# Optimization experiments

Hardware: AMD Instinct MI355X
Metric: run time of the kernel (lower is better)

The kernel has to match this reference:

```python
import jax, jax.numpy as jnp
import numpy as np

BATCH = 2048
SEQ_LEN = 8192


def setup_inputs() -> dict:
    key = jax.random.key(0)
    k1, k2 = jax.random.split(key)
    inputs = jax.random.normal(k1, (BATCH, SEQ_LEN), dtype=jnp.float32)
    filters = jax.random.normal(k2, (BATCH, SEQ_LEN), dtype=jnp.float32)
    return {"inputs": inputs, "filters": filters}


def reference(inputs, filters):
    # FFT-based long convolution with zero-padding to 2L (linear, not circular, conv).
    # torch norm='forward': rfft divides by n, irfft multiplies by n -> net scale 1/n.
    L = inputs.shape[-1]
    n = 2 * L  # rfft with n=2L implicitly zero-pads, same as F.pad then rfft
    x_f = jnp.fft.rfft(inputs, n=n, axis=-1, norm="forward")   # (B, L+1) complex
    h_f = jnp.fft.rfft(filters, n=n, axis=-1, norm="forward")  # (B, L+1) complex
    y = jnp.fft.irfft(x_f * h_f, n=n, axis=-1, norm="forward")  # (B, 2L)
    return y[..., :L]
```

## Files before the change

kernel.cpp:

```cpp
#include <hip/hip_runtime.h>

#define L_LEN 8192
#define N_FFT 16384
#define NB    1024

#define LB __launch_bounds__(NB)

typedef float f2 __attribute__((ext_vector_type(2)));

__device__ __forceinline__ f2 mkf2(float a, float b) { f2 v; v.x = a; v.y = b; return v; }

__device__ __forceinline__ f2 cmul(f2 a, f2 w) {
    return mkf2(a.y, a.y) * mkf2(-w.y, w.x) + mkf2(a.x, a.x) * w;
}

__host__ __device__ constexpr int swz(int i) {
    return i ^ ((((i) >> 4) ^ ((i) >> 8) ^ ((i) >> 12)) & 15);
}

__device__ __forceinline__ int rev4_12(int m) {
    int r = 0;
#pragma unroll
    for (int d = 0; d < 6; ++d) { r = (r << 2) | (m & 3); m >>= 2; }
    return r;
}

__device__ __forceinline__ void bfly_dif(f2& x0, f2& x1, f2& x2, f2& x3,
                                         f2 w1, f2 w2, f2 w3) {
    f2 A = x0 + x2, B = x0 - x2, C = x1 + x3, D = x1 - x3;
    f2 iD = mkf2(-D.y, D.x);
    x0 = A + C;
    x1 = cmul(B - iD, w1);
    x2 = cmul(A - C, w2);
    x3 = cmul(B + iD, w3);
}

__device__ __forceinline__ void bfly_dit(f2& x0, f2& x1, f2& x2, f2& x3,
                                         f2 w1, f2 w2, f2 w3) {
    f2 a1 = cmul(x1, w1), a2 = cmul(x2, w2), a3 = cmul(x3, w3);
    f2 E = x0 + a2, F = x0 - a2, G = a1 + a3, K = a1 - a3;
    f2 iK = mkf2(-K.y, K.x);
    x0 = E + G; x1 = F + iK; x2 = E - G; x3 = F - iK;
}

__device__ __forceinline__ void bfly_dif1(f2* z) {
    f2 A = z[0] + z[2], B = z[0] - z[2], C = z[1] + z[3], D = z[1] - z[3];
    f2 iD = mkf2(-D.y, D.x);
    z[0] = A + C; z[1] = B - iD; z[2] = A - C; z[3] = B + iD;
}
__device__ __forceinline__ void bfly_dit1(f2* z) {
    f2 E = z[0] + z[2], F = z[0] - z[2], G = z[1] + z[3], K = z[1] - z[3];
    f2 iK = mkf2(-K.y, K.x);
    z[0] = E + G; z[1] = F + iK; z[2] = E - G; z[3] = F - iK;
}

__device__ __forceinline__ void pointwise_pair(f2& Zm, f2& Zr) {
    f2 half = mkf2(0.5f, 0.5f);
    f2 X = half * (Zm + mkf2(Zr.x, -Zr.y));
    f2 H = half * (mkf2(Zm.y, -Zm.x) + mkf2(Zr.y, Zr.x));
    f2 Y = cmul(X, H);
    Zm = Y;
    Zr = mkf2(Y.x, -Y.y);
}

#define CT0 1.0f
#define CT1 0.92387953251128674f
#define CT2 0.70710678118654752f
#define CT3 0.38268343236508977f
#define ST1 0.38268343236508977f
#define ST2 0.70710678118654752f
#define ST3 0.92387953251128674f

template<int QA>
__device__ __forceinline__ void fwd_pair(f2* lds, int tid) {
    constexpr int QB = QA / 4;
    const int g = tid / QB;
    const int u = tid % QB;
    const int sb = swz(g * (4 * QA) + u);
    f2 r[4][4];
#pragma unroll
    for (int jA = 0; jA < 4; ++jA)
#pragma unroll
        for (int jB = 0; jB < 4; ++jB)
            r[jA][jB] = lds[sb ^ swz(jA * QA + jB * QB)];

    {
        const float angA = -6.283185307179586f / (float)(4 * QA);
        float sn, cs;
        __sincosf(angA * (float)u, &sn, &cs);
        f2 u1 = mkf2(cs, sn);
        const f2 lad[4] = {mkf2(CT0, 0.f), mkf2(CT1, -ST1), mkf2(CT2, -ST2), mkf2(CT3, -ST3)};
#pragma unroll
        for (int jB = 0; jB < 4; ++jB) {
            f2 w1 = (jB == 0) ? u1 : cmul(u1, lad[jB]);
            f2 w2 = cmul(w1, w1);
            f2 w3 = cmul(w2, w1);
            bfly_dif(r[0][jB], r[1][jB], r[2][jB], r[3][jB], w1, w2, w3);
        }
    }
    {
        const float angB = -6.283185307179586f / (float)(4 * QB);
        float sn, cs;
        __sincosf(angB * (float)u, &sn, &cs);
        f2 v1 = mkf2(cs, sn);
        f2 v2 = cmul(v1, v1);
        f2 v3 = cmul(v2, v1);
#pragma unroll
        for (int jA = 0; jA < 4; ++jA)
            bfly_dif(r[jA][0], r[jA][1], r[jA][2], r[jA][3], v1, v2, v3);
    }

#pragma unroll
    for (int jA = 0; jA < 4; ++jA)
#pragma unroll
        for (int jB = 0; jB < 4; ++jB)
            lds[sb ^ swz(jA * QA + jB * QB)] = r[jA][jB];
}

template<int QA>
__device__ __forceinline__ void inv_pair(f2* lds, int tid) {
    constexpr int QB = 4 * QA;
    const int G = tid / QA;
    const int u = tid % QA;
    const int sb = swz(G * (16 * QA) + u);
    f2 r[4][4];
#pragma unroll
    for (int jA = 0; jA < 4; ++jA)
#pragma unroll
        for (int jB = 0; jB < 4; ++jB)
            r[jA][jB] = lds[sb ^ swz(jA * QA + jB * QB)];

    {
        const float angA = 6.283185307179586f / (float)(4 * QA);
        float sn, cs;
        __sincosf(angA * (float)u, &sn, &cs);
        f2 a1 = mkf2(cs, sn);
        f2 a2 = cmul(a1, a1);
        f2 a3 = cmul(a2, a1);
#pragma unroll
        for (int jB = 0; jB < 4; ++jB)
            bfly_dit(r[0][jB], r[1][jB], r[2][jB], r[3][jB], a1, a2, a3);
    }
    {
        const float angB = 6.283185307179586f / (float)(4 * QB);
        float sn, cs;
        __sincosf(angB * (float)u, &sn, &cs);
        f2 b1 = mkf2(cs, sn);
        const f2 lad[4] = {mkf2(CT0, 0.f), mkf2(CT1, ST1), mkf2(CT2, ST2), mkf2(CT3, ST3)};
#pragma unroll
        for (int jA = 0; jA < 4; ++jA) {
            f2 w1 = (jA == 0) ? b1 : cmul(b1, lad[jA]);
            f2 w2 = cmul(w1, w1);
            f2 w3 = cmul(w2, w1);
            bfly_dit(r[jA][0], r[jA][1], r[jA][2], r[jA][3], w1, w2, w3);
        }
    }

#pragma unroll
    for (int jA = 0; jA < 4; ++jA)
#pragma unroll
        for (int jB = 0; jB < 4; ++jB)
            lds[sb ^ swz(jA * QA + jB * QB)] = r[jA][jB];
}

__global__ LB
void fftconv_kernel(const float* __restrict__ xin,
                    const float* __restrict__ hin,
                    float* __restrict__ out)
{
    __shared__ f2 lds[N_FFT];

    const int row = blockIdx.x;
    const int tid = threadIdx.x;
    const float* xr = xin + (size_t)row * L_LEN;
    const float* hr = hin + (size_t)row * L_LEN;

    const int s4t = swz(4 * tid);
#pragma unroll
    for (int iter = 0; iter < 2; ++iter) {
        float4 xv = ((const float4*)xr)[tid + iter * NB];
        float4 hv = ((const float4*)hr)[tid + iter * NB];
        lds[s4t ^ swz(iter * 4096 + 0)] = mkf2(xv.x, hv.x);
        lds[s4t ^ swz(iter * 4096 + 1)] = mkf2(xv.y, hv.y);
        lds[s4t ^ swz(iter * 4096 + 2)] = mkf2(xv.z, hv.z);
        lds[s4t ^ swz(iter * 4096 + 3)] = mkf2(xv.w, hv.w);
    }
    const int st = swz(tid);
#pragma unroll
    for (int it = 0; it < 8; ++it)
        lds[st ^ swz(8192 + it * 1024)] = mkf2(0.f, 0.f);
    __syncthreads();

    fwd_pair<4096>(lds, tid); __syncthreads();
    fwd_pair<256>(lds, tid);  __syncthreads();
    fwd_pair<16>(lds, tid);   __syncthreads();

#pragma unroll
    for (int iter = 0; iter < 2; ++iter) {
        const int p = tid + iter * NB;
        if (p == 0) {
            f2 z[4];
#pragma unroll
            for (int k = 0; k < 4; ++k) z[k] = lds[k];
            bfly_dif1(z);
            z[0] = mkf2(z[0].x * z[0].y, 0.f);
            z[2] = mkf2(z[2].x * z[2].y, 0.f);
            pointwise_pair(z[1], z[3]);
            bfly_dit1(z);
#pragma unroll
            for (int k = 0; k < 4; ++k) lds[k] = z[k];
            f2 w[4];
#pragma unroll
            for (int k = 0; k < 4; ++k) w[k] = lds[8 + k];
            bfly_dif1(w);
            pointwise_pair(w[0], w[3]);
            pointwise_pair(w[1], w[2]);
            bfly_dit1(w);
#pragma unroll
            for (int k = 0; k < 4; ++k) lds[8 + k] = w[k];
        } else {
            const int sA = swz(4 * rev4_12(p));
            const int sB = swz(4 * rev4_12(4096 - p));
            f2 A[4], B[4];
#pragma unroll
            for (int k = 0; k < 4; ++k) A[k] = lds[sA ^ k];
#pragma unroll
            for (int k = 0; k < 4; ++k) B[k] = lds[sB ^ k];
            bfly_dif1(A);
            bfly_dif1(B);
            pointwise_pair(A[0], B[3]);
            pointwise_pair(A[1], B[2]);
            pointwise_pair(A[2], B[1]);
            pointwise_pair(A[3], B[0]);
            bfly_dit1(A);
            bfly_dit1(B);
#pragma unroll
            for (int k = 0; k < 4; ++k) lds[sA ^ k] = A[k];
#pragma unroll
            for (int k = 0; k < 4; ++k) lds[sB ^ k] = B[k];
        }
    }
    __syncthreads();

    inv_pair<4>(lds, tid);    __syncthreads();
    inv_pair<64>(lds, tid);   __syncthreads();
    inv_pair<1024>(lds, tid); __syncthreads();

    const float scale = 1.0f / ((float)N_FFT * (float)N_FFT);
    float* orow = out + (size_t)row * L_LEN;
#pragma unroll
    for (int iter = 0; iter < 2; ++iter) {
        float4 o;
        o.x = lds[s4t ^ swz(iter * 4096 + 0)].x * scale;
        o.y = lds[s4t ^ swz(iter * 4096 + 1)].x * scale;
        o.z = lds[s4t ^ swz(iter * 4096 + 2)].x * scale;
        o.w = lds[s4t ^ swz(iter * 4096 + 3)].x * scale;
        ((float4*)orow)[tid + iter * NB] = o;
    }
}

extern "C" void kernel_launch(void* const* d_in, const int* in_sizes, int n_in,
                              void* d_out, int out_size, void* d_ws, size_t ws_size,
                              hipStream_t stream) {
    const float* x = (const float*)d_in[0];
    const float* h = (const float*)d_in[1];
    float* out = (float*)d_out;
    const int rows = in_sizes[0] / L_LEN;
    fftconv_kernel<<<dim3(rows), dim3(NB), 0, stream>>>(x, h, out);
}
```

Measured before the change: 126.6 us.

## Fuse global load/store into first/last FFT passes with 512-thread SoA layout

```diff
diff --git a/kernel.cpp b/kernel.cpp
--- a/kernel.cpp
+++ b/kernel.cpp
@@ -2,20 +2,38 @@
 
 #define L_LEN 8192
 #define N_FFT 16384
-#define NB    1024
-
-#define LB __launch_bounds__(NB)
+#define NB    512
+
+#define LB __launch_bounds__(NB, 2)
 
 typedef float f2 __attribute__((ext_vector_type(2)));
 
-__device__ __forceinline__ f2 mkf2(float a, float b) { f2 v; v.x = a; v.y = b; return v; }
-
-__device__ __forceinline__ f2 cmul(f2 a, f2 w) {
-    return mkf2(a.y, a.y) * mkf2(-w.y, w.x) + mkf2(a.x, a.x) * w;
-}
-
-__host__ __device__ constexpr int swz(int i) {
-    return i ^ ((((i) >> 4) ^ ((i) >> 8) ^ ((i) >> 12)) & 15);
+struct cpx { f2 re, im; };
+
+__device__ __forceinline__ f2 bc(float s) { f2 v; v.x = s; v.y = s; return v; }
+__device__ __forceinline__ f2 mk2(float a, float b) { f2 v; v.x = a; v.y = b; return v; }
+
+__device__ __forceinline__ cpx cadd(cpx a, cpx b) { return {a.re + b.re, a.im + b.im}; }
+__device__ __forceinline__ cpx csub(cpx a, cpx b) { return {a.re - b.re, a.im - b.im}; }
+__device__ __forceinline__ cpx cmul(cpx a, cpx w) {
+    return {a.re * w.re - a.im * w.im, a.re * w.im + a.im * w.re};
+}
+__device__ __forceinline__ cpx addmi(cpx a, cpx b) { return {a.re + b.im, a.im - b.re}; }
+__device__ __forceinline__ cpx addpi(cpx a, cpx b) { return {a.re - b.im, a.im + b.re}; }
+
+__host__ __device__ constexpr int wrd(int i) {
+    return ((i & ~31) << 1) | ((i ^ (i >> 5) ^ (i >> 10)) & 31);
+}
+
+__device__ __forceinline__ cpx ldsld(const float* lds, int wA, int wB) {
+    cpx v;
+    v.re.x = lds[wA];      v.re.y = lds[wB];
+    v.im.x = lds[wA ^ 32]; v.im.y = lds[wB ^ 32];
+    return v;
+}
+__device__ __forceinline__ void ldsst(float* lds, int wA, int wB, cpx v) {
+    lds[wA] = v.re.x;      lds[wB] = v.re.y;
+    lds[wA ^ 32] = v.im.x; lds[wB ^ 32] = v.im.y;
 }
 
 __device__ __forceinline__ int rev4_12(int m) {
@@ -25,45 +43,36 @@
     return r;
 }
 
-__device__ __forceinline__ void bfly_dif(f2& x0, f2& x1, f2& x2, f2& x3,
-                                         f2 w1, f2 w2, f2 w3) {
-    f2 A = x0 + x2, B = x0 - x2, C = x1 + x3, D = x1 - x3;
-    f2 iD = mkf2(-D.y, D.x);
-    x0 = A + C;
-    x1 = cmul(B - iD, w1);
-    x2 = cmul(A - C, w2);
-    x3 = cmul(B + iD, w3);
-}
-
-__device__ __forceinline__ void bfly_dit(f2& x0, f2& x1, f2& x2, f2& x3,
-                                         f2 w1, f2 w2, f2 w3) {
-    f2 a1 = cmul(x1, w1), a2 = cmul(x2, w2), a3 = cmul(x3, w3);
-    f2 E = x0 + a2, F = x0 - a2, G = a1 + a3, K = a1 - a3;
-    f2 iK = mkf2(-K.y, K.x);
-    x0 = E + G; x1 = F + iK; x2 = E - G; x3 = F - iK;
-}
-
-__device__ __forceinline__ void bfly_dif1(f2* z) {
-    f2 A = z[0] + z[2], B = z[0] - z[2], C = z[1] + z[3], D = z[1] - z[3];
-    f2 iD = mkf2(-D.y, D.x);
-    z[0] = A + C; z[1] = B - iD; z[2] = A - C; z[3] = B + iD;
-}
-__device__ __forceinline__ void bfly_dit1(f2* z) {
-    f2 E = z[0] + z[2], F = z[0] - z[2], G = z[1] + z[3], K = z[1] - z[3];
-    f2 iK = mkf2(-K.y, K.x);
-    z[0] = E + G; z[1] = F + iK; z[2] = E - G; z[3] = F - iK;
-}
-
-__device__ __forceinline__ void pointwise_pair(f2& Zm, f2& Zr) {
-    f2 half = mkf2(0.5f, 0.5f);
-    f2 X = half * (Zm + mkf2(Zr.x, -Zr.y));
-    f2 H = half * (mkf2(Zm.y, -Zm.x) + mkf2(Zr.y, Zr.x));
-    f2 Y = cmul(X, H);
-    Zm = Y;
-    Zr = mkf2(Y.x, -Y.y);
-}
-
-#define CT0 1.0f
+__device__ __forceinline__ void bfly_dif(cpx& x0, cpx& x1, cpx& x2, cpx& x3,
+                                         cpx w1, cpx w2, cpx w3) {
+    cpx A = cadd(x0, x2), B = csub(x0, x2), C = cadd(x1, x3), D = csub(x1, x3);
+    x0 = cadd(A, C);
+    x1 = cmul(addmi(B, D), w1);
+    x2 = cmul(csub(A, C), w2);
+    x3 = cmul(addpi(B, D), w3);
+}
+__device__ __forceinline__ void bfly_dit(cpx& x0, cpx& x1, cpx& x2, cpx& x3,
+                                         cpx w1, cpx w2, cpx w3) {
+    cpx a1 = cmul(x1, w1), a2 = cmul(x2, w2), a3 = cmul(x3, w3);
+    cpx E = cadd(x0, a2), F = csub(x0, a2), G = cadd(a1, a3), K = csub(a1, a3);
+    x0 = cadd(E, G); x1 = addpi(F, K); x2 = csub(E, G); x3 = addmi(F, K);
+}
+__device__ __forceinline__ void bfly_dif1(cpx* z) {
+    cpx A = cadd(z[0], z[2]), B = csub(z[0], z[2]), C = cadd(z[1], z[3]), D = csub(z[1], z[3]);
+    z[0] = cadd(A, C); z[1] = addmi(B, D); z[2] = csub(A, C); z[3] = addpi(B, D);
+}
+__device__ __forceinline__ void bfly_dit1(cpx* z) {
+    cpx E = cadd(z[0], z[2]), F = csub(z[0], z[2]), G = cadd(z[1], z[3]), K = csub(z[1], z[3]);
+    z[0] = cadd(E, G); z[1] = addpi(F, K); z[2] = csub(E, G); z[3] = addmi(F, K);
+}
+__device__ __forceinline__ void pw(cpx& Zm, cpx& Zr) {
+    f2 h = bc(0.5f);
+    cpx X{h * (Zm.re + Zr.re), h * (Zm.im - Zr.im)};
+    cpx H{h * (Zm.im + Zr.im), h * (Zr.re - Zm.re)};
+    cpx Y = cmul(X, H);
+    Zm = Y; Zr = {Y.re, -Y.im};
+}
+
 #define CT1 0.92387953251128674f
 #define CT2 0.70710678118654752f
 #define CT3 0.38268343236508977f
@@ -71,96 +80,238 @@
 #define ST2 0.70710678118654752f
 #define ST3 0.92387953251128674f
 
+__device__ __forceinline__ void fwd_first(float* lds, int tid,
+                                          const float* __restrict__ xr,
+                                          const float* __restrict__ hr) {
+    const cpx ladf[4] = {{bc(1.f), bc(0.f)}, {bc(CT1), bc(-ST1)},
+                         {bc(CT2), bc(-ST2)}, {bc(CT3), bc(-ST3)}};
+    cpx r[4][4];
+    float sn, cs;
+    __sincosf(-6.283185307179586f / 16384.f * (float)tid, &sn, &cs);
+    const float KAc = 0.98078528040323044913f, KAs = -0.19509032201612826785f;
+    float csb = cs * KAc - sn * KAs, snb = cs * KAs + sn * KAc;
+    cpx u1{mk2(cs, csb), mk2(sn, snb)};
+#pragma unroll
+    for (int jB = 0; jB < 4; ++jB) {
+        const int t = tid + jB * 1024;
+        cpx z0{mk2(xr[t], xr[t + 512]), mk2(hr[t], hr[t + 512])};
+        cpx z1{mk2(xr[t + 4096], xr[t + 4608]), mk2(hr[t + 4096], hr[t + 4608])};
+        cpx w1 = (jB == 0) ? u1 : cmul(u1, ladf[jB]);
+        cpx w2 = cmul(w1, w1), w3 = cmul(w2, w1);
+        r[0][jB] = cadd(z0, z1);
+        r[1][jB] = cmul(addmi(z0, z1), w1);
+        r[2][jB] = cmul(csub(z0, z1), w2);
+        r[3][jB] = cmul(addpi(z0, z1), w3);
+    }
+    __sincosf(-6.283185307179586f / 4096.f * (float)tid, &sn, &cs);
+    const float KBc = 0.70710678118654752f, KBs = -0.70710678118654752f;
+    float csb2 = cs * KBc - sn * KBs, snb2 = cs * KBs + sn * KBc;
+    cpx v1{mk2(cs, csb2), mk2(sn, snb2)};
+    cpx v2 = cmul(v1, v1), v3 = cmul(v2, v1);
+#pragma unroll
+    for (int jA = 0; jA < 4; ++jA)
+        bfly_dif(r[jA][0], r[jA][1], r[jA][2], r[jA][3], v1, v2, v3);
+    const int wb = wrd(tid);
+#pragma unroll
+    for (int jA = 0; jA < 4; ++jA)
+#pragma unroll
+        for (int jB = 0; jB < 4; ++jB) {
+            const int wA = wb ^ wrd(jA * 4096 + jB * 1024);
+            ldsst(lds, wA, wA ^ 1040, r[jA][jB]);
+        }
+}
+
 template<int QA>
-__device__ __forceinline__ void fwd_pair(f2* lds, int tid) {
+__device__ __forceinline__ void fwd_pair(float* lds, int tid) {
     constexpr int QB = QA / 4;
-    const int g = tid / QB;
-    const int u = tid % QB;
-    const int sb = swz(g * (4 * QA) + u);
-    f2 r[4][4];
-#pragma unroll
-    for (int jA = 0; jA < 4; ++jA)
-#pragma unroll
-        for (int jB = 0; jB < 4; ++jB)
-            r[jA][jB] = lds[sb ^ swz(jA * QA + jB * QB)];
-
-    {
-        const float angA = -6.283185307179586f / (float)(4 * QA);
-        float sn, cs;
-        __sincosf(angA * (float)u, &sn, &cs);
-        f2 u1 = mkf2(cs, sn);
-        const f2 lad[4] = {mkf2(CT0, 0.f), mkf2(CT1, -ST1), mkf2(CT2, -ST2), mkf2(CT3, -ST3)};
-#pragma unroll
-        for (int jB = 0; jB < 4; ++jB) {
-            f2 w1 = (jB == 0) ? u1 : cmul(u1, lad[jB]);
-            f2 w2 = cmul(w1, w1);
-            f2 w3 = cmul(w2, w1);
-            bfly_dif(r[0][jB], r[1][jB], r[2][jB], r[3][jB], w1, w2, w3);
-        }
-    }
-    {
-        const float angB = -6.283185307179586f / (float)(4 * QB);
-        float sn, cs;
-        __sincosf(angB * (float)u, &sn, &cs);
-        f2 v1 = mkf2(cs, sn);
-        f2 v2 = cmul(v1, v1);
-        f2 v3 = cmul(v2, v1);
-#pragma unroll
-        for (int jA = 0; jA < 4; ++jA)
-            bfly_dif(r[jA][0], r[jA][1], r[jA][2], r[jA][3], v1, v2, v3);
-    }
-
-#pragma unroll
-    for (int jA = 0; jA < 4; ++jA)
-#pragma unroll
-        for (int jB = 0; jB < 4; ++jB)
-            lds[sb ^ swz(jA * QA + jB * QB)] = r[jA][jB];
+    const cpx ladf[4] = {{bc(1.f), bc(0.f)}, {bc(CT1), bc(-ST1)},
+                         {bc(CT2), bc(-ST2)}, {bc(CT3), bc(-ST3)}};
+    const int g = tid / QB, u = tid % QB;
+    const int wb = wrd(g * (4 * QA) + u);
+    cpx r[4][4];
+#pragma unroll
+    for (int jA = 0; jA < 4; ++jA)
+#pragma unroll
+        for (int jB = 0; jB < 4; ++jB) {
+            const int wA = wb ^ wrd(jA * QA + jB * QB);
+            r[jA][jB] = ldsld(lds, wA, wA ^ 16392);
+        }
+    float sn, cs;
+    __sincosf(-6.283185307179586f / (float)(4 * QA) * (float)u, &sn, &cs);
+    cpx u1{bc(cs), bc(sn)};
+#pragma unroll
+    for (int jB = 0; jB < 4; ++jB) {
+        cpx w1 = (jB == 0) ? u1 : cmul(u1, ladf[jB]);
+        cpx w2 = cmul(w1, w1), w3 = cmul(w2, w1);
+        bfly_dif(r[0][jB], r[1][jB], r[2][jB], r[3][jB], w1, w2, w3);
+    }
+    __sincosf(-6.283185307179586f / (float)(4 * QB) * (float)u, &sn, &cs);
+    cpx v1{bc(cs), bc(sn)}, v2 = cmul(v1, v1), v3 = cmul(v2, v1);
+#pragma unroll
+    for (int jA = 0; jA < 4; ++jA)
+        bfly_dif(r[jA][0], r[jA][1], r[jA][2], r[jA][3], v1, v2, v3);
+#pragma unroll
+    for (int jA = 0; jA < 4; ++jA)
+#pragma unroll
+        for (int jB = 0; jB < 4; ++jB) {
+            const int wA = wb ^ wrd(jA * QA + jB * QB);
+            ldsst(lds, wA, wA ^ 16392, r[jA][jB]);
+        }
 }
 
 template<int QA>
-__device__ __forceinline__ void inv_pair(f2* lds, int tid) {
+__device__ __forceinline__ void inv_pair(float* lds, int tid) {
     constexpr int QB = 4 * QA;
-    const int G = tid / QA;
-    const int u = tid % QA;
-    const int sb = swz(G * (16 * QA) + u);
-    f2 r[4][4];
-#pragma unroll
-    for (int jA = 0; jA < 4; ++jA)
-#pragma unroll
-        for (int jB = 0; jB < 4; ++jB)
-            r[jA][jB] = lds[sb ^ swz(jA * QA + jB * QB)];
-
-    {
-        const float angA = 6.283185307179586f / (float)(4 * QA);
-        float sn, cs;
-        __sincosf(angA * (float)u, &sn, &cs);
-        f2 a1 = mkf2(cs, sn);
-        f2 a2 = cmul(a1, a1);
-        f2 a3 = cmul(a2, a1);
-#pragma unroll
-        for (int jB = 0; jB < 4; ++jB)
-            bfly_dit(r[0][jB], r[1][jB], r[2][jB], r[3][jB], a1, a2, a3);
-    }
-    {
-        const float angB = 6.283185307179586f / (float)(4 * QB);
-        float sn, cs;
-        __sincosf(angB * (float)u, &sn, &cs);
-        f2 b1 = mkf2(cs, sn);
-        const f2 lad[4] = {mkf2(CT0, 0.f), mkf2(CT1, ST1), mkf2(CT2, ST2), mkf2(CT3, ST3)};
-#pragma unroll
-        for (int jA = 0; jA < 4; ++jA) {
-            f2 w1 = (jA == 0) ? b1 : cmul(b1, lad[jA]);
-            f2 w2 = cmul(w1, w1);
-            f2 w3 = cmul(w2, w1);
-            bfly_dit(r[jA][0], r[jA][1], r[jA][2], r[jA][3], w1, w2, w3);
-        }
-    }
-
-#pragma unroll
-    for (int jA = 0; jA < 4; ++jA)
-#pragma unroll
-        for (int jB = 0; jB < 4; ++jB)
-            lds[sb ^ swz(jA * QA + jB * QB)] = r[jA][jB];
+    const cpx ladi[4] = {{bc(1.f), bc(0.f)}, {bc(CT1), bc(ST1)},
+                         {bc(CT2), bc(ST2)}, {bc(CT3), bc(ST3)}};
+    const int G = tid / QA, u = tid % QA;
+    const int wb = wrd(G * (16 * QA) + u);
+    cpx r[4][4];
+#pragma unroll
+    for (int jA = 0; jA < 4; ++jA)
+#pragma unroll
+        for (int jB = 0; jB < 4; ++jB) {
+            const int wA = wb ^ wrd(jA * QA + jB * QB);
+            r[jA][jB] = ldsld(lds, wA, wA ^ 16392);
+        }
+    float sn, cs;
+    __sincosf(6.283185307179586f / (float)(4 * QA) * (float)u, &sn, &cs);
+    cpx a1{bc(cs), bc(sn)}, a2 = cmul(a1, a1), a3 = cmul(a2, a1);
+#pragma unroll
+    for (int jB = 0; jB < 4; ++jB)
+        bfly_dit(r[0][jB], r[1][jB], r[2][jB], r[3][jB], a1, a2, a3);
+    __sincosf(6.283185307179586f / (float)(4 * QB) * (float)u, &sn, &cs);
+    cpx b1{bc(cs), bc(sn)};
+#pragma unroll
+    for (int jA = 0; jA < 4; ++jA) {
+        cpx w1 = (jA == 0) ? b1 : cmul(b1, ladi[jA]);
+        cpx w2 = cmul(w1, w1), w3 = cmul(w2, w1);
+        bfly_dit(r[jA][0], r[jA][1], r[jA][2], r[jA][3], w1, w2, w3);
+    }
+#pragma unroll
+    for (int jA = 0; jA < 4; ++jA)
+#pragma unroll
+        for (int jB = 0; jB < 4; ++jB) {
+            const int wA = wb ^ wrd(jA * QA + jB * QB);
+            ldsst(lds, wA, wA ^ 16392, r[jA][jB]);
+        }
+}
+
+__device__ __forceinline__ void inv_last(const float* lds, int tid,
+                                         float* __restrict__ orow) {
+    const cpx ladi[4] = {{bc(1.f), bc(0.f)}, {bc(CT1), bc(ST1)},
+                         {bc(CT2), bc(ST2)}, {bc(CT3), bc(ST3)}};
+    const int wb = wrd(tid);
+    cpx r[4][4];
+#pragma unroll
+    for (int jA = 0; jA < 4; ++jA)
+#pragma unroll
+        for (int jB = 0; jB < 4; ++jB) {
+            const int wA = wb ^ wrd(jA * 1024 + jB * 4096);
+            r[jA][jB] = ldsld(lds, wA, wA ^ 1040);
+        }
+    float sn, cs;
+    __sincosf(6.283185307179586f / 4096.f * (float)tid, &sn, &cs);
+    const float PC4 = 0.70710678118654752f, PS4 = 0.70710678118654752f;
+    float csb = cs * PC4 - sn * PS4, snb = cs * PS4 + sn * PC4;
+    cpx a1{mk2(cs, csb), mk2(sn, snb)}, a2 = cmul(a1, a1), a3 = cmul(a2, a1);
+#pragma unroll
+    for (int jB = 0; jB < 4; ++jB)
+        bfly_dit(r[0][jB], r[1][jB], r[2][jB], r[3][jB], a1, a2, a3);
+    __sincosf(6.283185307179586f / 16384.f * (float)tid, &sn, &cs);
+    const float PC16 = 0.98078528040323044913f, PS16 = 0.19509032201612826785f;
+    float csb2 = cs * PC16 - sn * PS16, snb2 = cs * PS16 + sn * PC16;
+    cpx b1{mk2(cs, csb2), mk2(sn, snb2)};
+    const f2 sc = bc(1.0f / (16384.f * 16384.f));
+#pragma unroll
+    for (int jA = 0; jA < 4; ++jA) {
+        cpx w1 = (jA == 0) ? b1 : cmul(b1, ladi[jA]);
+        cpx w2 = cmul(w1, w1), w3 = cmul(w2, w1);
+        cpx x0 = r[jA][0];
+        cpx A1 = cmul(r[jA][1], w1);
+        f2  A2re = r[jA][2].re * w2.re - r[jA][2].im * w2.im;
+        cpx A3 = cmul(r[jA][3], w3);
+        f2 y0 = (x0.re + A2re + A1.re + A3.re) * sc;
+        f2 y1 = (x0.re - A2re - A1.im + A3.im) * sc;
+        orow[tid + jA * 1024]              = y0.x;
+        orow[tid + 512 + jA * 1024]        = y0.y;
+        orow[tid + jA * 1024 + 4096]       = y1.x;
+        orow[tid + 512 + jA * 1024 + 4096] = y1.y;
+    }
+}
+
+__device__ __forceinline__ void combo_pair(float* lds, int p0, int p1) {
+    const int wA0 = wrd(4 * rev4_12(p0)), wA1 = wrd(4 * rev4_12(p1));
+    const int wB0 = wrd(4 * rev4_12(4096 - p0)), wB1 = wrd(4 * rev4_12(4096 - p1));
+    cpx A[4], B[4];
+#pragma unroll
+    for (int k = 0; k < 4; ++k) {
+        A[k] = ldsld(lds, wA0 ^ k, wA1 ^ k);
+        B[k] = ldsld(lds, wB0 ^ k, wB1 ^ k);
+    }
+    bfly_dif1(A); bfly_dif1(B);
+    pw(A[0], B[3]); pw(A[1], B[2]); pw(A[2], B[1]); pw(A[3], B[0]);
+    bfly_dit1(A); bfly_dit1(B);
+#pragma unroll
+    for (int k = 0; k < 4; ++k) {
+        ldsst(lds, wA0 ^ k, wA1 ^ k, A[k]);
+        ldsst(lds, wB0 ^ k, wB1 ^ k, B[k]);
+    }
+}
+
+struct c1 { float re, im; };
+__device__ __forceinline__ c1 ld1(const float* lds, int w) { return {lds[w], lds[w ^ 32]}; }
+__device__ __forceinline__ void st1(float* lds, int w, c1 v) { lds[w] = v.re; lds[w ^ 32] = v.im; }
+__device__ __forceinline__ void s_dif1(c1* z) {
+    float Ar = z[0].re + z[2].re, Ai = z[0].im + z[2].im;
+    float Br = z[0].re - z[2].re, Bi = z[0].im - z[2].im;
+    float Cr = z[1].re + z[3].re, Ci = z[1].im + z[3].im;
+    float Dr = z[1].re - z[3].re, Di = z[1].im - z[3].im;
+    z[0] = {Ar + Cr, Ai + Ci}; z[1] = {Br + Di, Bi - Dr};
+    z[2] = {Ar - Cr, Ai - Ci}; z[3] = {Br - Di, Bi + Dr};
+}
+__device__ __forceinline__ void s_dit1(c1* z) {
+    float Er = z[0].re + z[2].re, Ei = z[0].im + z[2].im;
+    float Fr = z[0].re - z[2].re, Fi = z[0].im - z[2].im;
+    float Gr = z[1].re + z[3].re, Gi = z[1].im + z[3].im;
+    float Kr = z[1].re - z[3].re, Ki = z[1].im - z[3].im;
+    z[0] = {Er + Gr, Ei + Gi}; z[1] = {Fr - Ki, Fi + Kr};
+    z[2] = {Er - Gr, Ei - Gi}; z[3] = {Fr + Ki, Fi - Kr};
+}
+__device__ __forceinline__ void s_pw(c1& a, c1& b) {
+    float Xr = 0.5f * (a.re + b.re), Xi = 0.5f * (a.im - b.im);
+    float Hr = 0.5f * (a.im + b.im), Hi = 0.5f * (b.re - a.re);
+    float Yr = Xr * Hr - Xi * Hi, Yi = Xr * Hi + Xi * Hr;
+    a = {Yr, Yi}; b = {Yr, -Yi};
+}
+__device__ void combo_special(float* lds) {
+    c1 z[4];
+#pragma unroll
+    for (int k = 0; k < 4; ++k) z[k] = ld1(lds, k);
+    s_dif1(z);
+    z[0] = {z[0].re * z[0].im, 0.f};
+    z[2] = {z[2].re * z[2].im, 0.f};
+    s_pw(z[1], z[3]);
+    s_dit1(z);
+#pragma unroll
+    for (int k = 0; k < 4; ++k) st1(lds, k, z[k]);
+    c1 w[4];
+#pragma unroll
+    for (int k = 0; k < 4; ++k) w[k] = ld1(lds, 8 + k);
+    s_dif1(w);
+    s_pw(w[0], w[3]); s_pw(w[1], w[2]);
+    s_dit1(w);
+#pragma unroll
+    for (int k = 0; k < 4; ++k) st1(lds, 8 + k, w[k]);
+    const int wA = wrd(4 * rev4_12(512)), wB = wrd(4 * rev4_12(3584));
+    c1 A[4], Bq[4];
+#pragma unroll
+    for (int k = 0; k < 4; ++k) { A[k] = ld1(lds, wA ^ k); Bq[k] = ld1(lds, wB ^ k); }
+    s_dif1(A); s_dif1(Bq);
+    s_pw(A[0], Bq[3]); s_pw(A[1], Bq[2]); s_pw(A[2], Bq[1]); s_pw(A[3], Bq[0]);
+    s_dit1(A); s_dit1(Bq);
+#pragma unroll
+    for (int k = 0; k < 4; ++k) { st1(lds, wA ^ k, A[k]); st1(lds, wB ^ k, Bq[k]); }
 }
 
 __global__ LB
@@ -168,95 +319,25 @@
                     const float* __restrict__ hin,
                     float* __restrict__ out)
 {
-    __shared__ f2 lds[N_FFT];
+    __shared__ float lds[2 * N_FFT];
 
     const int row = blockIdx.x;
     const int tid = threadIdx.x;
     const float* xr = xin + (size_t)row * L_LEN;
     const float* hr = hin + (size_t)row * L_LEN;
 
-    const int s4t = swz(4 * tid);
-#pragma unroll
-    for (int iter = 0; iter < 2; ++iter) {
-        float4 xv = ((const float4*)xr)[tid + iter * NB];
-        float4 hv = ((const float4*)hr)[tid + iter * NB];
-        lds[s4t ^ swz(iter * 4096 + 0)] = mkf2(xv.x, hv.x);
-        lds[s4t ^ swz(iter * 4096 + 1)] = mkf2(xv.y, hv.y);
-        lds[s4t ^ swz(iter * 4096 + 2)] = mkf2(xv.z, hv.z);
-        lds[s4t ^ swz(iter * 4096 + 3)] = mkf2(xv.w, hv.w);
-    }
-    const int st = swz(tid);
-#pragma unroll
-    for (int it = 0; it < 8; ++it)
-        lds[st ^ swz(8192 + it * 1024)] = mkf2(0.f, 0.f);
+    fwd_first(lds, tid, xr, hr); __syncthreads();
+    fwd_pair<256>(lds, tid);     __syncthreads();
+    fwd_pair<16>(lds, tid);      __syncthreads();
+
+    if (tid == 0) combo_special(lds);
+    else          combo_pair(lds, tid, tid + 512);
+    combo_pair(lds, tid + 1024, tid + 1536);
     __syncthreads();
 
-    fwd_pair<4096>(lds, tid); __syncthreads();
-    fwd_pair<256>(lds, tid);  __syncthreads();
-    fwd_pair<16>(lds, tid);   __syncthreads();
-
-#pragma unroll
-    for (int iter = 0; iter < 2; ++iter) {
-        const int p = tid + iter * NB;
-        if (p == 0) {
-            f2 z[4];
-#pragma unroll
-            for (int k = 0; k < 4; ++k) z[k] = lds[k];
-            bfly_dif1(z);
-            z[0] = mkf2(z[0].x * z[0].y, 0.f);
-            z[2] = mkf2(z[2].x * z[2].y, 0.f);
-            pointwise_pair(z[1], z[3]);
-            bfly_dit1(z);
-#pragma unroll
-            for (int k = 0; k < 4; ++k) lds[k] = z[k];
-            f2 w[4];
-#pragma unroll
-            for (int k = 0; k < 4; ++k) w[k] = lds[8 + k];
-            bfly_dif1(w);
-            pointwise_pair(w[0], w[3]);
-            pointwise_pair(w[1], w[2]);
-            bfly_dit1(w);
-#pragma unroll
-            for (int k = 0; k < 4; ++k) lds[8 + k] = w[k];
-        } else {
-            const int sA = swz(4 * rev4_12(p));
-            const int sB = swz(4 * rev4_12(4096 - p));
-            f2 A[4], B[4];
-#pragma unroll
-            for (int k = 0; k < 4; ++k) A[k] = lds[sA ^ k];
-#pragma unroll
-            for (int k = 0; k < 4; ++k) B[k] = lds[sB ^ k];
-            bfly_dif1(A);
-            bfly_dif1(B);
-            pointwise_pair(A[0], B[3]);
-            pointwise_pair(A[1], B[2]);
-            pointwise_pair(A[2], B[1]);
-            pointwise_pair(A[3], B[0]);
-            bfly_dit1(A);
-            bfly_dit1(B);
-#pragma unroll
-            for (int k = 0; k < 4; ++k) lds[sA ^ k] = A[k];
-#pragma unroll
-            for (int k = 0; k < 4; ++k) lds[sB ^ k] = B[k];
-        }
-    }
-    __syncthreads();
-
-    inv_pair<4>(lds, tid);    __syncthreads();
-    inv_pair<64>(lds, tid);   __syncthreads();
-    inv_pair<1024>(lds, tid); __syncthreads();
-
-    const float scale = 1.0f / ((float)N_FFT * (float)N_FFT);
-    float* orow = out + (size_t)row * L_LEN;
-#pragma unroll
-    for (int iter = 0; iter < 2; ++iter) {
-        float4 o;
-        o.x = lds[s4t ^ swz(iter * 4096 + 0)].x * scale;
-        o.y = lds[s4t ^ swz(iter * 4096 + 1)].x * scale;
-        o.z = lds[s4t ^ swz(iter * 4096 + 2)].x * scale;
-        o.w = lds[s4t ^ swz(iter * 4096 + 3)].x * scale;
-        ((float4*)orow)[tid + iter * NB] = o;
-    }
+    inv_pair<4>(lds, tid);  __syncthreads();
+    inv_pair<64>(lds, tid); __syncthreads();
+    inv_last(lds, tid, out + (size_t)row * L_LEN);
 }
 
 extern "C" void kernel_launch(void* const* d_in, const int* in_sizes, int n_in,
```

After: 137.9 us. 1.09x slower.
